# Kernel tuning notes

Measured on AMD Instinct MI355X. Metric: run time of the kernel, lower is better.

Reference implementation:

```python
import jax, jax.numpy as jnp
import numpy as np

N_HEADS, INPUT_DIM, EMBED_DIM = 8, 128, 128
KEY_DIM = EMBED_DIM // N_HEADS  # val_dim = key_dim = 16
B, N = 8, 1024


def setup_inputs() -> dict:
    key = jax.random.key(0)
    ks = jax.random.split(key, 16)
    stdv_k = 1.0 / np.sqrt(KEY_DIM)
    stdv_e = 1.0 / np.sqrt(EMBED_DIM)

    def U(k, shape, s):
        return jax.random.uniform(k, shape, jnp.float32, -s, s)

    hdk = (N_HEADS, INPUT_DIM, KEY_DIM)
    hke = (N_HEADS, KEY_DIM, EMBED_DIM)
    return {
        "q_n": jax.random.normal(ks[0], (B, N, INPUT_DIM), jnp.float32),
        "q_c": jax.random.normal(ks[1], (B, N, INPUT_DIM), jnp.float32),
        "mask": jax.random.bernoulli(ks[2], 0.5, (B, N, N)),
        "W_query_n": U(ks[3], hdk, stdv_k),
        "W_key_nn": U(ks[4], hdk, stdv_k),
        "W_val_nn": U(ks[5], hdk, stdv_k),
        "W_key_c": U(ks[6], hdk, stdv_k),
        "W_val_c": U(ks[7], hdk, stdv_k),
        "W_query_c": U(ks[8], hdk, stdv_k),
        "W_key_n": U(ks[9], hdk, stdv_k),
        "W_val_n": U(ks[10], hdk, stdv_k),
        "W_out_node": U(ks[11], hke, stdv_e),
        "W_out_color": U(ks[12], hke, stdv_e),
    }


def reference(q_n, q_c, mask, W_query_n, W_key_nn, W_val_nn, W_key_c, W_val_c,
              W_query_c, W_key_n, W_val_n, W_out_node, W_out_color):
    norm = 1.0 / jnp.sqrt(jnp.asarray(KEY_DIM, q_n.dtype))
    neg_inf = jnp.asarray(-jnp.inf, q_n.dtype)

    def proj(x, W):  # (B,N,D), (H,D,K) -> (H,B,N,K)
        return jnp.einsum('bnd,hdk->hbnk', x, W)

    # --- color stream: q_c attends over nodes q_n ---
    Q_c = proj(q_c, W_query_c)
    K_n = proj(q_n, W_key_n)
    V_n = proj(q_n, W_val_n)
    attn_c = jax.nn.softmax(norm * jnp.einsum('hbqk,hbnk->hbqn', Q_c, K_n), axis=-1)
    heads_c = jnp.einsum('hbqn,hbnv->hbqv', attn_c, V_n)
    out_color = jnp.einsum('hbqv,hve->bqe', heads_c, W_out_color)

    # --- node stream: masked self-attention + attention over colors ---
    Q_n = proj(q_n, W_query_n)
    K_nn = proj(q_n, W_key_nn)
    V_nn = proj(q_n, W_val_nn)
    comp_nn = norm * jnp.einsum('hbqk,hbnk->hbqn', Q_n, K_nn)
    m = mask[None]  # (1,B,Q,N) broadcast over heads; True = not allowed
    comp_nn = jnp.where(m, neg_inf, comp_nn)
    attn_nn = jax.nn.softmax(comp_nn, axis=-1)
    attn_nn = jnp.where(m, jnp.asarray(0.0, q_n.dtype), attn_nn)
    heads_nn = jnp.einsum('hbqn,hbnv->hbqv', attn_nn, V_nn)

    K_nc = proj(q_c, W_key_c)
    V_nc = proj(q_c, W_val_c)
    attn_nc = jax.nn.softmax(norm * jnp.einsum('hbqk,hbnk->hbqn', Q_n, K_nc), axis=-1)
    heads_nc = jnp.einsum('hbqn,hbnv->hbqv', attn_nc, V_nc)

    heads = heads_nn + heads_nc
    out = jnp.einsum('hbqv,hve->bqe', heads, W_out_node)
    return (out, out_color)
```

## Files before the change

### kernel.cpp

```cpp
#include <hip/hip_runtime.h>
#include <stdint.h>

#define NH 8
#define NB 8
#define NN 1024
#define ND 128
#define NK 16
#define NF (NB*NN)
#define C2EXP 0.36067376022224085f
#define LSTR 136

typedef float f32x16 __attribute__((ext_vector_type(16)));
typedef short bf16x8 __attribute__((ext_vector_type(8)));

__device__ __forceinline__ uint16_t f2bf(float f){
  uint32_t x = __float_as_uint(f);
  uint32_t r = (x + 0x7fffu + ((x>>16)&1u)) >> 16;
  return (uint16_t)r;
}
__device__ __forceinline__ float fast_exp2(float x){
#if __has_builtin(__builtin_amdgcn_exp2f)
  return __builtin_amdgcn_exp2f(x);
#else
  return exp2f(x);
#endif
}

__global__ __launch_bounds__(256) void pack_kernel(const int* __restrict__ mask,
                                                   uint32_t* __restrict__ packN,
                                                   uint16_t* __restrict__ onesw){
  if (blockIdx.x == 0) {
    for (int i = threadIdx.x; i < 1024; i += 256) onesw[i] = 0x3F80;
  }
  const int w = threadIdx.x >> 6, lane = threadIdx.x & 63;
  const int row = blockIdx.x*4 + w;
  const int* mp = mask + (size_t)row*NN;
  uint32_t* dst = packN + (size_t)row*32;
  for (int wq = 0; wq < 16; ++wq) {
    int v = mp[wq*64 + lane];
    unsigned long long bal = __ballot(v != 0);
    if (lane == 0) { dst[wq*2] = (uint32_t)bal; dst[wq*2+1] = (uint32_t)(bal>>32); }
  }
}

struct ProjArgs { const float* x[8]; const float* w[8]; };

__global__ __launch_bounds__(512, 4) void proj_kernel(ProjArgs args, uint16_t* ws){
  __shared__ __align__(16) uint16_t WT[128*LSTR];
  __shared__ __align__(16) uint16_t S[128*LSTR];
  const int p = blockIdx.y;
  const int rb = blockIdx.x;
  const int tid = threadIdx.x;

  const float4* w4 = (const float4*)args.w[p];
  #pragma unroll
  for (int i = 0; i < 8; ++i) {
    int e4 = i*512 + tid;
    float4 f = w4[e4];
    int e = e4*4;
    int h = e >> 11, d = (e >> 4) & 127, k = e & 15;
    uint16_t* wr = &WT[(h*16 + k)*LSTR + d];
    wr[0*LSTR] = f2bf(f.x); wr[1*LSTR] = f2bf(f.y);
    wr[2*LSTR] = f2bf(f.z); wr[3*LSTR] = f2bf(f.w);
  }
  __syncthreads();

  const int wave = tid >> 6, lane = tid & 63;
  const int l5 = lane >> 5, lm = lane & 31;
  const int rt = wave & 3, nh2 = wave >> 2;
  const int r0 = rb*128 + rt*32;
  const float* xrow = args.x[p] + (size_t)(r0 + lm)*ND + l5*8;

  bf16x8 afr[8];
  #pragma unroll
  for (int kt = 0; kt < 8; ++kt) {
    float4 f0 = *(const float4*)(xrow + kt*16);
    float4 f1 = *(const float4*)(xrow + kt*16 + 4);
    bf16x8 a;
    a[0]=f2bf(f0.x); a[1]=f2bf(f0.y); a[2]=f2bf(f0.z); a[3]=f2bf(f0.w);
    a[4]=f2bf(f1.x); a[5]=f2bf(f1.y); a[6]=f2bf(f1.z); a[7]=f2bf(f1.w);
    afr[kt] = a;
  }

  const bool tr = (p==2)|(p==5)|(p==7);
  const float qsc = (p==0 || p==3) ? C2EXP : 1.0f;
  #pragma unroll
  for (int nt2 = 0; nt2 < 2; ++nt2) {
    const int nt = nh2*2 + nt2;
    f32x16 acc;
    #pragma unroll
    for (int i = 0; i < 16; ++i) acc[i] = 0.f;
    #pragma unroll
    for (int kt = 0; kt < 8; ++kt) {
      bf16x8 b = *(const bf16x8*)(&WT[(nt*32 + lm)*LSTR + kt*16 + l5*8]);
      acc = __builtin_amdgcn_mfma_f32_32x32x16_bf16(afr[kt], b, acc, 0, 0, 0);
    }
    #pragma unroll
    for (int i = 0; i < 16; ++i) {
      int r = rt*32 + (i&3) + 8*(i>>2) + 4*l5;
      int c = nt*32 + lm;
      if (tr) {
        int t2 = (r>>2)&3;
        int rp = (t2==1 || t2==2) ? (r^12) : r;
        S[c*LSTR + rp] = f2bf(acc[i]);
      } else {
        S[r*LSTR + c] = f2bf(acc[i]*qsc);
      }
    }
  }
  __syncthreads();

  uint16_t* dst = ws + (size_t)p*((size_t)NH*NF*NK);
  if (!tr) {
    #pragma unroll
    for (int it = 0; it < 4; ++it) {
      int c = it*512 + tid;
      int row = c >> 4, cg = c & 15;
      bf16x8 v = *(const bf16x8*)(&S[row*LSTR + cg*8]);
      int h = cg >> 1, k8 = cg & 1;
      *(bf16x8*)(dst + ((size_t)h*NF + rb*128 + row)*NK + k8*8) = v;
    }
  } else {
    const int b = rb >> 3, nb = (rb & 7)*128;
    #pragma unroll
    for (int it = 0; it < 4; ++it) {
      int c = it*512 + tid;
      int col = c >> 4, ng = c & 15;
      bf16x8 v = *(const bf16x8*)(&S[col*LSTR + ng*8]);
      int h = col >> 4, k = col & 15;
      *(bf16x8*)(dst + ((size_t)(h*NB + b)*NK + k)*NN + nb + ng*8) = v;
    }
  }
}

template<bool MASKED>
__device__ __forceinline__ void attn_stream(
    const uint4* __restrict__ kbuf, bf16x8 aq,
    const uint16_t* __restrict__ vbase, const uint4* __restrict__ pmw4,
    int nh, int l5, int lm, f32x16& O)
{
  f32x16 Z;
  #pragma unroll
  for (int i = 0; i < 16; ++i) Z[i] = 0.f;

  uint32_t mw[16];
  if (MASKED) {
    uint4 m0 = pmw4[nh*4+0], m1 = pmw4[nh*4+1];
    uint4 m2 = pmw4[nh*4+2], m3 = pmw4[nh*4+3];
    mw[0]=m0.x; mw[1]=m0.y; mw[2]=m0.z; mw[3]=m0.w;
    mw[4]=m1.x; mw[5]=m1.y; mw[6]=m1.z; mw[7]=m1.w;
    mw[8]=m2.x; mw[9]=m2.y; mw[10]=m2.z; mw[11]=m2.w;
    mw[12]=m3.x; mw[13]=m3.y; mw[14]=m3.z; mw[15]=m3.w;
  }

  const int base_n = nh*512;
  const bool vload = (lm < 17);

  bf16x8 av1, av2, av1n, av2n;
  #pragma unroll
  for (int i = 0; i < 8; ++i) { av1[i]=0; av2[i]=0; av1n[i]=0; av2n[i]=0; }
  if (vload) {
    const uint16_t* vp = vbase + base_n + l5*8;
    av1 = *(const bf16x8*)(vp);
    av2 = *(const bf16x8*)(vp + 16);
  }
  f32x16 Stc = __builtin_amdgcn_mfma_f32_32x32x16_bf16(
      *(const bf16x8*)(&kbuf[l5*1024 + base_n + lm]), aq, Z, 0, 0, 0);

  #pragma unroll
  for (int t = 0; t < 16; ++t) {
    f32x16 Stn;
    if (t < 15) {
      const int n1 = base_n + (t+1)*32;
      if (vload) {
        const uint16_t* vp = vbase + n1 + l5*8;
        av1n = *(const bf16x8*)(vp);
        av2n = *(const bf16x8*)(vp + 16);
      }
      Stn = __builtin_amdgcn_mfma_f32_32x32x16_bf16(
          *(const bf16x8*)(&kbuf[l5*1024 + n1 + lm]), aq, Z, 0, 0, 0);
    }

    const uint32_t mws = MASKED ? (mw[t] >> (4*l5)) : 0u;
    float p[16];
    #pragma unroll
    for (int i = 0; i < 16; ++i) {
      float pv = fast_exp2(Stc[i]);
      if (MASKED && ((mws >> ((i&3) + 8*(i>>2))) & 1u)) pv = 0.f;
      p[i] = pv;
    }
    union { uint32_t u[4]; bf16x8 v; } B1, B2;
    #pragma unroll
    for (int k = 0; k < 4; ++k) {
      B1.u[k] = __builtin_amdgcn_perm(__float_as_uint(p[2*k+1]),
                                      __float_as_uint(p[2*k]),   0x07060302u);
      B2.u[k] = __builtin_amdgcn_perm(__float_as_uint(p[2*k+9]),
                                      __float_as_uint(p[2*k+8]), 0x07060302u);
    }
    O = __builtin_amdgcn_mfma_f32_32x32x16_bf16(av1, B1.v, O, 0, 0, 0);
    O = __builtin_amdgcn_mfma_f32_32x32x16_bf16(av2, B2.v, O, 0, 0, 0);

    if (t < 15) { Stc = Stn; av1 = av1n; av2 = av2n; }
  }
}

__global__ __launch_bounds__(256, 4) void attn_kernel(
    const uint16_t* __restrict__ Qn_, const uint16_t* __restrict__ Knn,
    const uint16_t* __restrict__ VTnn, const uint16_t* __restrict__ Knc,
    const uint16_t* __restrict__ VTnc,
    const uint16_t* __restrict__ Qc_, const uint16_t* __restrict__ Kn,
    const uint16_t* __restrict__ VTn,
    const uint32_t* __restrict__ packN, const uint16_t* __restrict__ onesb,
    uint16_t* __restrict__ hnn_, uint16_t* __restrict__ hnc_,
    uint16_t* __restrict__ hc_)
{
  __shared__ uint4 kbuf[2048];
  const int z = blockIdx.z;
  const uint16_t* Q  = (z == 2) ? Qc_ : Qn_;
  const uint16_t* K  = (z == 0) ? Knn : (z == 1) ? Knc : Kn;
  const uint16_t* VT = (z == 0) ? VTnn : (z == 1) ? VTnc : VTn;
  uint16_t* outp     = (z == 0) ? hnn_ : (z == 1) ? hnc_ : hc_;

  const int h = blockIdx.x >> 3, b = blockIdx.x & 7;
  const int hb = h*8 + b;
  const size_t base = ((size_t)h*NF + (size_t)b*NN)*NK;
  const int tid = threadIdx.x;

  const uint4* k1 = (const uint4*)(K + base);
  for (int i = tid; i < 2048; i += 256)
    kbuf[(i & 1)*1024 + (i >> 1)] = k1[i];
  __syncthreads();

  const int wave = tid >> 6, lane = tid & 63;
  const int l5 = lane >> 5, lm = lane & 31;
  const int qt = wave & 1, nh = wave >> 1;
  const int q = blockIdx.y*64 + qt*32 + lm;

  const bf16x8 aq = *(const bf16x8*)(Q + base + (size_t)q*NK + l5*8);
  const uint4* pmw4 = (const uint4*)(packN + ((size_t)b*NN + q)*32);

  const uint16_t* VTb = VT + (size_t)hb*(NK*NN);
  const uint16_t* vb = (lm < 16) ? (VTb + (size_t)lm*NN) : onesb;

  f32x16 O;
  #pragma unroll
  for (int i = 0; i < 16; ++i) O[i] = 0.f;

  if (z == 0) attn_stream<true >(kbuf, aq, vb, pmw4,   nh, l5, lm, O);
  else        attn_stream<false>(kbuf, aq, vb, nullptr, nh, l5, lm, O);

  float L1 = O[8] + __shfl_xor(O[8], 32, 64);

  __syncthreads();
  float* cw = ((float*)kbuf) + (size_t)((qt*2 + l5)*32 + lm)*9;
  if (nh == 1) {
    #pragma unroll
    for (int i = 0; i < 8; ++i) cw[i] = O[i];
    cw[8] = L1;
  }
  __syncthreads();
  if (nh == 0) {
    const float l1 = L1 + cw[8];
    const float i1 = (l1 > 0.f) ? 1.f/l1 : 0.f;
    uint32_t w[4];
    #pragma unroll
    for (int k = 0; k < 4; ++k) {
      float va = (O[2*k]   + cw[2*k])  *i1;
      float vb2 = (O[2*k+1] + cw[2*k+1])*i1;
      w[k] = ((uint32_t)f2bf(vb2) << 16) | f2bf(va);
    }
    uint16_t* hp = outp + ((size_t)b*NN + q)*128 + h*16 + l5*4;
    *(uint2*)(hp)     = make_uint2(w[0], w[1]);
    *(uint2*)(hp + 8) = make_uint2(w[2], w[3]);
  }
}

__global__ __launch_bounds__(512, 4) void outproj_kernel(
    const uint16_t* __restrict__ hnn, const uint16_t* __restrict__ hnc,
    const uint16_t* __restrict__ hc,
    const float* __restrict__ wn, const float* __restrict__ wc,
    float* __restrict__ out)
{
  __shared__ __align__(16) uint16_t WT[128*LSTR];
  const int s = blockIdx.y;
  const int rb = blockIdx.x;
  const int tid = threadIdx.x;
  const float* wsrc = s ? wc : wn;
  const float4* w4 = (const float4*)wsrc;
  #pragma unroll
  for (int i = 0; i < 8; ++i) {
    int e4 = i*512 + tid;
    float4 f = w4[e4];
    int e = e4*4;
    int c = e >> 7, col = e & 127;
    uint16_t* wr = &WT[col*LSTR + c];
    wr[0*LSTR] = f2bf(f.x); wr[1*LSTR] = f2bf(f.y);
    wr[2*LSTR] = f2bf(f.z); wr[3*LSTR] = f2bf(f.w);
  }
  __syncthreads();

  const int wave = tid >> 6, lane = tid & 63;
  const int l5 = lane >> 5, lm = lane & 31;
  const int rt = wave >> 2, nt = wave & 3;
  const int r0 = rb*64 + rt*32;
  const size_t hoff = (size_t)(r0 + lm)*128 + l5*8;
  const uint16_t* hp1 = (s ? hc : hnn) + hoff;
  bf16x8 afr[8], afr2[8];
  #pragma unroll
  for (int kt = 0; kt < 8; ++kt) afr[kt] = *(const bf16x8*)(hp1 + kt*16);
  if (!s) {
    const uint16_t* hp2 = hnc + hoff;
    #pragma unroll
    for (int kt = 0; kt < 8; ++kt) afr2[kt] = *(const bf16x8*)(hp2 + kt*16);
  }

  float* dst = out + (size_t)s*((size_t)NF*ND) + (size_t)r0*ND;
  f32x16 acc;
  #pragma unroll
  for (int i = 0; i < 16; ++i) acc[i] = 0.f;
  #pragma unroll
  for (int kt = 0; kt < 8; ++kt) {
    bf16x8 b = *(const bf16x8*)(&WT[(nt*32 + lm)*LSTR + kt*16 + l5*8]);
    acc = __builtin_amdgcn_mfma_f32_32x32x16_bf16(afr[kt], b, acc, 0, 0, 0);
    if (!s) acc = __builtin_amdgcn_mfma_f32_32x32x16_bf16(afr2[kt], b, acc, 0, 0, 0);
  }
  #pragma unroll
  for (int i = 0; i < 16; ++i) {
    int r = (i&3) + 8*(i>>2) + 4*l5;
    dst[(size_t)r*ND + nt*32 + lm] = acc[i];
  }
}

extern "C" void kernel_launch(void* const* d_in, const int* in_sizes, int n_in,
                              void* d_out, int out_size, void* d_ws, size_t ws_size,
                              hipStream_t stream)
{
  const float* q_n = (const float*)d_in[0];
  const float* q_c = (const float*)d_in[1];
  const int* mask = (const int*)d_in[2];
  const float* W[10];
  for (int i = 0; i < 10; ++i) W[i] = (const float*)d_in[3+i];

  uint16_t* ws16 = (uint16_t*)d_ws;
  const size_t PE = (size_t)NH*NF*NK;
  uint16_t* Qc   = ws16 + 0*PE;
  uint16_t* Kn   = ws16 + 1*PE;
  uint16_t* VTn  = ws16 + 2*PE;
  uint16_t* Qn   = ws16 + 3*PE;
  uint16_t* Knn  = ws16 + 4*PE;
  uint16_t* VTnn = ws16 + 5*PE;
  uint16_t* Knc  = ws16 + 6*PE;
  uint16_t* VTnc = ws16 + 7*PE;
  uint16_t* hnn  = ws16 + 8*PE;
  uint32_t* packN   = (uint32_t*)(ws16 + 9*PE);
  uint16_t* onesb   = ws16 + 9*PE + 524288;
  uint16_t* hc   = ws16 + 10*PE;
  uint16_t* hnc  = ws16 + 11*PE;

  pack_kernel<<<2048, 256, 0, stream>>>(mask, packN, onesb);

  ProjArgs pa;
  pa.x[0]=q_c; pa.w[0]=W[5];
  pa.x[1]=q_n; pa.w[1]=W[6];
  pa.x[2]=q_n; pa.w[2]=W[7];
  pa.x[3]=q_n; pa.w[3]=W[0];
  pa.x[4]=q_n; pa.w[4]=W[1];
  pa.x[5]=q_n; pa.w[5]=W[2];
  pa.x[6]=q_c; pa.w[6]=W[3];
  pa.x[7]=q_c; pa.w[7]=W[4];
  proj_kernel<<<dim3(64, 8), 512, 0, stream>>>(pa, ws16);

  attn_kernel<<<dim3(64, 16, 3), 256, 0, stream>>>(
      Qn, Knn, VTnn, Knc, VTnc, Qc, Kn, VTn, packN, onesb,
      hnn, hnc, hc);

  outproj_kernel<<<dim3(128, 2), 512, 0, stream>>>(hnn, hnc, hc,
                                                   W[8], W[9], (float*)d_out);
}
```

Before: 168.8 us.

## Stream K fragments directly from global memory instead of staging in LDS

Drops the LDS staging of the whole K tile and its barrier. Each wave now loads its K fragment straight from global memory, prefetching one step ahead, and reads mask words in groups of four instead of preloading all 16. This cuts LDS use and register pressure, and the launch bound rises to 5 blocks per CU for more occupancy. In exchange it adds global/L2 load latency inside the loop, loses the software pipelining of the score MFMA, and the two waves sharing a key range fetch K redundantly.

```diff
diff --git a/kernel.cpp b/kernel.cpp
--- a/kernel.cpp
+++ b/kernel.cpp
@@ -135,7 +135,7 @@
 
 template<bool MASKED>
 __device__ __forceinline__ void attn_stream(
-    const uint4* __restrict__ kbuf, bf16x8 aq,
+    const uint16_t* __restrict__ kp, bf16x8 aq,
     const uint16_t* __restrict__ vbase, const uint4* __restrict__ pmw4,
     int nh, int l5, int lm, f32x16& O)
 {
@@ -143,68 +143,66 @@
   #pragma unroll
   for (int i = 0; i < 16; ++i) Z[i] = 0.f;
 
-  uint32_t mw[16];
-  if (MASKED) {
-    uint4 m0 = pmw4[nh*4+0], m1 = pmw4[nh*4+1];
-    uint4 m2 = pmw4[nh*4+2], m3 = pmw4[nh*4+3];
-    mw[0]=m0.x; mw[1]=m0.y; mw[2]=m0.z; mw[3]=m0.w;
-    mw[4]=m1.x; mw[5]=m1.y; mw[6]=m1.z; mw[7]=m1.w;
-    mw[8]=m2.x; mw[9]=m2.y; mw[10]=m2.z; mw[11]=m2.w;
-    mw[12]=m3.x; mw[13]=m3.y; mw[14]=m3.z; mw[15]=m3.w;
-  }
-
   const int base_n = nh*512;
   const bool vload = (lm < 17);
-
-  bf16x8 av1, av2, av1n, av2n;
-  #pragma unroll
-  for (int i = 0; i < 8; ++i) { av1[i]=0; av2[i]=0; av1n[i]=0; av2n[i]=0; }
-  if (vload) {
-    const uint16_t* vp = vbase + base_n + l5*8;
-    av1 = *(const bf16x8*)(vp);
-    av2 = *(const bf16x8*)(vp + 16);
-  }
-  f32x16 Stc = __builtin_amdgcn_mfma_f32_32x32x16_bf16(
-      *(const bf16x8*)(&kbuf[l5*1024 + base_n + lm]), aq, Z, 0, 0, 0);
+  const uint16_t* kl = kp + (size_t)(base_n + lm)*NK + l5*8;
+  const uint16_t* vl = vbase + base_n + l5*8;
+
+  bf16x8 kf_c = *(const bf16x8*)(kl);
+  bf16x8 kf_n;
+  uint4 mq, mqn;
+  if (MASKED) { mq = pmw4[nh*4]; mqn = mq; }
+
+  bf16x8 av1, av2;
+  #pragma unroll
+  for (int i = 0; i < 8; ++i) { av1[i]=0; av2[i]=0; }
 
   #pragma unroll
   for (int t = 0; t < 16; ++t) {
-    f32x16 Stn;
-    if (t < 15) {
-      const int n1 = base_n + (t+1)*32;
-      if (vload) {
-        const uint16_t* vp = vbase + n1 + l5*8;
-        av1n = *(const bf16x8*)(vp);
-        av2n = *(const bf16x8*)(vp + 16);
+    if (vload) {
+      const uint16_t* vp = vl + t*32;
+      av1 = *(const bf16x8*)(vp);
+      av2 = *(const bf16x8*)(vp + 16);
+    }
+    if (t < 15) kf_n = *(const bf16x8*)(kl + (t+1)*512);
+    if (MASKED && (t&3)==0 && t < 12) mqn = pmw4[nh*4 + (t>>2) + 1];
+
+    f32x16 St = __builtin_amdgcn_mfma_f32_32x32x16_bf16(kf_c, aq, Z, 0, 0, 0);
+
+    uint32_t mws = 0u;
+    if (MASKED) {
+      uint32_t w = ((t&3)==0) ? mq.x : ((t&3)==1) ? mq.y
+                 : ((t&3)==2) ? mq.z : mq.w;
+      mws = w >> (4*l5);
+    }
+    union { uint32_t u[4]; bf16x8 v; } B1, B2;
+    #pragma unroll
+    for (int k = 0; k < 4; ++k) {
+      float p0 = fast_exp2(St[2*k]);
+      float p1 = fast_exp2(St[2*k+1]);
+      float p8 = fast_exp2(St[2*k+8]);
+      float p9 = fast_exp2(St[2*k+9]);
+      if (MASKED) {
+        const int i0 = 2*k, i1 = 2*k+1, i8 = 2*k+8, i9 = 2*k+9;
+        if ((mws >> ((i0&3) + 8*(i0>>2))) & 1u) p0 = 0.f;
+        if ((mws >> ((i1&3) + 8*(i1>>2))) & 1u) p1 = 0.f;
+        if ((mws >> ((i8&3) + 8*(i8>>2))) & 1u) p8 = 0.f;
+        if ((mws >> ((i9&3) + 8*(i9>>2))) & 1u) p9 = 0.f;
       }
-      Stn = __builtin_amdgcn_mfma_f32_32x32x16_bf16(
-          *(const bf16x8*)(&kbuf[l5*1024 + n1 + lm]), aq, Z, 0, 0, 0);
-    }
-
-    const uint32_t mws = MASKED ? (mw[t] >> (4*l5)) : 0u;
-    float p[16];
-    #pragma unroll
-    for (int i = 0; i < 16; ++i) {
-      float pv = fast_exp2(Stc[i]);
-      if (MASKED && ((mws >> ((i&3) + 8*(i>>2))) & 1u)) pv = 0.f;
-      p[i] = pv;
-    }
-    union { uint32_t u[4]; bf16x8 v; } B1, B2;
-    #pragma unroll
-    for (int k = 0; k < 4; ++k) {
-      B1.u[k] = __builtin_amdgcn_perm(__float_as_uint(p[2*k+1]),
-                                      __float_as_uint(p[2*k]),   0x07060302u);
-      B2.u[k] = __builtin_amdgcn_perm(__float_as_uint(p[2*k+9]),
-                                      __float_as_uint(p[2*k+8]), 0x07060302u);
+      B1.u[k] = __builtin_amdgcn_perm(__float_as_uint(p1),
+                                      __float_as_uint(p0), 0x07060302u);
+      B2.u[k] = __builtin_amdgcn_perm(__float_as_uint(p9),
+                                      __float_as_uint(p8), 0x07060302u);
     }
     O = __builtin_amdgcn_mfma_f32_32x32x16_bf16(av1, B1.v, O, 0, 0, 0);
     O = __builtin_amdgcn_mfma_f32_32x32x16_bf16(av2, B2.v, O, 0, 0, 0);
 
-    if (t < 15) { Stc = Stn; av1 = av1n; av2 = av2n; }
-  }
-}
-
-__global__ __launch_bounds__(256, 4) void attn_kernel(
+    kf_c = kf_n;
+    if (MASKED && (t&3)==3) mq = mqn;
+  }
+}
+
+__global__ __launch_bounds__(256, 5) void attn_kernel(
     const uint16_t* __restrict__ Qn_, const uint16_t* __restrict__ Knn,
     const uint16_t* __restrict__ VTnn, const uint16_t* __restrict__ Knc,
     const uint16_t* __restrict__ VTnc,
@@ -214,7 +212,7 @@
     uint16_t* __restrict__ hnn_, uint16_t* __restrict__ hnc_,
     uint16_t* __restrict__ hc_)
 {
-  __shared__ uint4 kbuf[2048];
+  __shared__ float cw[1152];
   const int z = blockIdx.z;
   const uint16_t* Q  = (z == 2) ? Qc_ : Qn_;
   const uint16_t* K  = (z == 0) ? Knn : (z == 1) ? Knc : Kn;
@@ -226,11 +224,6 @@
   const size_t base = ((size_t)h*NF + (size_t)b*NN)*NK;
   const int tid = threadIdx.x;
 
-  const uint4* k1 = (const uint4*)(K + base);
-  for (int i = tid; i < 2048; i += 256)
-    kbuf[(i & 1)*1024 + (i >> 1)] = k1[i];
-  __syncthreads();
-
   const int wave = tid >> 6, lane = tid & 63;
   const int l5 = lane >> 5, lm = lane & 31;
   const int qt = wave & 1, nh = wave >> 1;
@@ -246,27 +239,26 @@
   #pragma unroll
   for (int i = 0; i < 16; ++i) O[i] = 0.f;
 
-  if (z == 0) attn_stream<true >(kbuf, aq, vb, pmw4,   nh, l5, lm, O);
-  else        attn_stream<false>(kbuf, aq, vb, nullptr, nh, l5, lm, O);
+  if (z == 0) attn_stream<true >(K + base, aq, vb, pmw4,   nh, l5, lm, O);
+  else        attn_stream<false>(K + base, aq, vb, nullptr, nh, l5, lm, O);
 
   float L1 = O[8] + __shfl_xor(O[8], 32, 64);
 
-  __syncthreads();
-  float* cw = ((float*)kbuf) + (size_t)((qt*2 + l5)*32 + lm)*9;
+  float* cwp = cw + (size_t)((qt*2 + l5)*32 + lm)*9;
   if (nh == 1) {
     #pragma unroll
-    for (int i = 0; i < 8; ++i) cw[i] = O[i];
-    cw[8] = L1;
+    for (int i = 0; i < 8; ++i) cwp[i] = O[i];
+    cwp[8] = L1;
   }
   __syncthreads();
   if (nh == 0) {
-    const float l1 = L1 + cw[8];
+    const float l1 = L1 + cwp[8];
     const float i1 = (l1 > 0.f) ? 1.f/l1 : 0.f;
     uint32_t w[4];
     #pragma unroll
     for (int k = 0; k < 4; ++k) {
-      float va = (O[2*k]   + cw[2*k])  *i1;
-      float vb2 = (O[2*k+1] + cw[2*k+1])*i1;
+      float va = (O[2*k]   + cwp[2*k])  *i1;
+      float vb2 = (O[2*k+1] + cwp[2*k+1])*i1;
       w[k] = ((uint32_t)f2bf(vb2) << 16) | f2bf(va);
     }
     uint16_t* hp = outp + ((size_t)b*NN + q)*128 + h*16 + l5*4;
```

After: 168.8 us. About the same (-0.0%).
